# Kernel optimization log

Hardware: AMD Instinct MI355X
Metric: run time of the kernel (lower is better)

Reference implementation:

```python
import jax, jax.numpy as jnp
import numpy as np

N_NODES = 10000
IN_CH = 128
OUT_CH = 128
N_EDGES = 320000


def setup_inputs() -> dict:
    key = jax.random.key(0)
    k1, k2, k3, k4 = jax.random.split(key, 4)
    x = jax.random.normal(k1, (N_NODES, IN_CH), dtype=jnp.float32)
    edge_index = jax.random.randint(k2, (N_EDGES, 2), 0, N_NODES, dtype=jnp.int64)
    # Linear weights (torch stores [out, in]); scale like kaiming-uniform-ish
    w = jax.random.normal(k3, (OUT_CH, IN_CH), dtype=jnp.float32) / np.sqrt(IN_CH)
    b = jax.random.normal(k4, (OUT_CH, IN_CH), dtype=jnp.float32) / np.sqrt(IN_CH)
    return {"x": x, "edge_index": edge_index, "w": w, "b": b}


def reference(x, edge_index, w, b):
    n = x.shape[0]
    # Each edge (i, j) contributes x[j] to node i and x[i] to node j (undirected).
    src = jnp.concatenate([edge_index[:, 1], edge_index[:, 0]])  # feature source
    dst = jnp.concatenate([edge_index[:, 0], edge_index[:, 1]])  # aggregation target
    # segment-sum of gathered neighbor features -> [n, in_ch]
    agg_sum = jax.ops.segment_sum(x[src], dst, num_segments=n)
    deg = jax.ops.segment_sum(jnp.ones_like(dst, dtype=x.dtype), dst, num_segments=n)
    # mean with zero fallback for isolated nodes (original uses zeros vector)
    agg = jnp.where(deg[:, None] > 0, agg_sum / jnp.maximum(deg, 1.0)[:, None], 0.0)
    # out = ReLU(agg @ w^T + x @ b^T)
    return jax.nn.relu(agg @ w.T + x @ b.T)
```

## Files before the change

kernel.cpp:

```cpp
#include <hip/hip_runtime.h>

#define N_NODES 10000
#define CH 128
#define N_EDGES 320000
#define CAP 128
#define CSTR 16

#define NSLICE 8
#define FILL_CHUNKS (N_EDGES / 256)
#define FILL_BLOCKS (FILL_CHUNKS * NSLICE)
#define CONV_THREADS (N_NODES * CH / 8)
#define CONV_BLOCKS ((CONV_THREADS + 255) / 256)
#define PACK_THREADS (128 * 128)
#define PACK_BLOCKS (PACK_THREADS / 256)
#define KSEG 5
#define WBK (KSEG * CH)


typedef __attribute__((ext_vector_type(8))) short short8v;
typedef __attribute__((ext_vector_type(4))) float floatx4;

__device__ __forceinline__ unsigned short f2bf(float f) {
    unsigned u = __float_as_uint(f);
    return (unsigned short)((u + 0x7FFFu + ((u >> 16) & 1u)) >> 16);
}
__device__ __forceinline__ float bf2f(unsigned short h) {
    return __uint_as_float(((unsigned)h) << 16);
}

__global__ __launch_bounds__(256) void fill_conv_pack_kernel(const int* __restrict__ ei,
                                                             int* __restrict__ cursor,
                                                             unsigned short* __restrict__ adj,
                                                             const float* __restrict__ x,
                                                             unsigned short* __restrict__ xhi,
                                                             unsigned short* __restrict__ xlo,
                                                             const float* __restrict__ w,
                                                             const float* __restrict__ b,
                                                             unsigned short* __restrict__ wbt)
{
    const int bid = blockIdx.x;
    if (bid < FILL_BLOCKS) {
        const int slice = bid & (NSLICE - 1);
        const int chunk = bid >> 3;
        const int t = chunk * 256 + threadIdx.x;
        const int2 p = ((const int2*)ei)[t];
        const int a = p.x, c = p.y;
        const bool aok = (unsigned)a < N_NODES && (unsigned)c < N_NODES;
        if (aok && (a & 7) == slice) {
            const int s0 = atomicAdd(&cursor[a * CSTR], 1);
            if (s0 < CAP) adj[(size_t)a * CAP + s0] = (unsigned short)c;
        }
        if (aok && (c & 7) == slice) {
            const int s1 = atomicAdd(&cursor[c * CSTR], 1);
            if (s1 < CAP) adj[(size_t)c * CAP + s1] = (unsigned short)a;
        }
    } else if (bid < FILL_BLOCKS + CONV_BLOCKS) {
        const int t = (bid - FILL_BLOCKS) * 256 + threadIdx.x;
        const float4 a = ((const float4*)x)[t * 2];
        const float4 c = ((const float4*)x)[t * 2 + 1];
        ushort4 h0, h1, l0, l1;
        h0.x = f2bf(a.x); l0.x = f2bf(a.x - bf2f(h0.x));
        h0.y = f2bf(a.y); l0.y = f2bf(a.y - bf2f(h0.y));
        h0.z = f2bf(a.z); l0.z = f2bf(a.z - bf2f(h0.z));
        h0.w = f2bf(a.w); l0.w = f2bf(a.w - bf2f(h0.w));
        h1.x = f2bf(c.x); l1.x = f2bf(c.x - bf2f(h1.x));
        h1.y = f2bf(c.y); l1.y = f2bf(c.y - bf2f(h1.y));
        h1.z = f2bf(c.z); l1.z = f2bf(c.z - bf2f(h1.z));
        h1.w = f2bf(c.w); l1.w = f2bf(c.w - bf2f(h1.w));
        ((ushort4*)xhi)[t * 2]     = h0;
        ((ushort4*)xhi)[t * 2 + 1] = h1;
        ((ushort4*)xlo)[t * 2]     = l0;
        ((ushort4*)xlo)[t * 2 + 1] = l1;
    } else {
        const int t = (bid - FILL_BLOCKS - CONV_BLOCKS) * 256 + threadIdx.x;
        const int n = t >> 7;
        const int k = t & 127;
        const float wv = w[n * CH + k];
        const float bv = b[n * CH + k];
        const unsigned short whi = f2bf(wv);
        const unsigned short wlo = f2bf(wv - bf2f(whi));
        const unsigned short bhi = f2bf(bv);
        const unsigned short blo = f2bf(bv - bf2f(bhi));
        unsigned short* row = wbt + (size_t)n * WBK;
        row[k]          = whi;
        row[CH + k]     = wlo;
        row[2 * CH + k] = bhi;
        row[3 * CH + k] = blo;
        row[4 * CH + k] = bhi;
    }
}

__global__ __launch_bounds__(256) void gather_kernel(const unsigned short* __restrict__ xhi,
                                                     const int* __restrict__ cursor,
                                                     const unsigned short* __restrict__ adj,
                                                     unsigned short* __restrict__ aggb)
{
    const int wv   = threadIdx.x >> 6;
    const int node = blockIdx.x * 4 + wv;
    const int lane = threadIdx.x & 63;
    const int h    = lane >> 4;
    const int l    = lane & 15;

    const int deg = cursor[node * CSTR];
    const int d   = deg < CAP ? deg : CAP;
    const unsigned short* nb = adj + (size_t)node * CAP;

    float4 accA = {0.f, 0.f, 0.f, 0.f};
    float4 accB = {0.f, 0.f, 0.f, 0.f};
    const int nit = (d + 3) >> 2;
#pragma unroll 4
    for (int it = 0; it < nit; ++it) {
        const int idx = 4 * it + h;
        int j = nb[idx];
        j = j < N_NODES ? j : 0;
        const uint4 q = ((const uint4*)(xhi + (size_t)j * CH))[l];
        const float m = idx < d ? 1.0f : 0.0f;
        accA.x += m * __uint_as_float(q.x << 16);
        accA.y += m * __uint_as_float(q.x & 0xffff0000u);
        accA.z += m * __uint_as_float(q.y << 16);
        accA.w += m * __uint_as_float(q.y & 0xffff0000u);
        accB.x += m * __uint_as_float(q.z << 16);
        accB.y += m * __uint_as_float(q.z & 0xffff0000u);
        accB.z += m * __uint_as_float(q.w << 16);
        accB.w += m * __uint_as_float(q.w & 0xffff0000u);
    }
    accA.x += __shfl_xor(accA.x, 16, 64);
    accA.y += __shfl_xor(accA.y, 16, 64);
    accA.z += __shfl_xor(accA.z, 16, 64);
    accA.w += __shfl_xor(accA.w, 16, 64);
    accB.x += __shfl_xor(accB.x, 16, 64);
    accB.y += __shfl_xor(accB.y, 16, 64);
    accB.z += __shfl_xor(accB.z, 16, 64);
    accB.w += __shfl_xor(accB.w, 16, 64);
    accA.x += __shfl_xor(accA.x, 32, 64);
    accA.y += __shfl_xor(accA.y, 32, 64);
    accA.z += __shfl_xor(accA.z, 32, 64);
    accA.w += __shfl_xor(accA.w, 32, 64);
    accB.x += __shfl_xor(accB.x, 32, 64);
    accB.y += __shfl_xor(accB.y, 32, 64);
    accB.z += __shfl_xor(accB.z, 32, 64);
    accB.w += __shfl_xor(accB.w, 32, 64);

    if (h == 0) {
        const float inv = deg > 0 ? 1.0f / (float)deg : 0.0f;
        uint4 o;
        o.x = (unsigned)f2bf(accA.x * inv) | ((unsigned)f2bf(accA.y * inv) << 16);
        o.y = (unsigned)f2bf(accA.z * inv) | ((unsigned)f2bf(accA.w * inv) << 16);
        o.z = (unsigned)f2bf(accB.x * inv) | ((unsigned)f2bf(accB.y * inv) << 16);
        o.w = (unsigned)f2bf(accB.z * inv) | ((unsigned)f2bf(accB.w * inv) << 16);
        ((uint4*)(aggb + (size_t)node * CH))[l] = o;
    }
}

__global__ __launch_bounds__(256) void mfma_gemm_kernel(const unsigned short* __restrict__ aggb,
                                                        const unsigned short* __restrict__ xhi,
                                                        const unsigned short* __restrict__ xlo,
                                                        const unsigned short* __restrict__ wbt,
                                                        float* __restrict__ out)
{
    const int wv    = threadIdx.x >> 6;
    const int lane  = threadIdx.x & 63;
    const int W     = blockIdx.x * 4 + wv;
    const int mtile = W >> 3;
    const int n0    = (W & 7) * 16;
    const int r     = lane & 15;
    const int q     = lane >> 4;
    const int arow  = mtile * 16 + r;

    const unsigned short* brow = wbt + (size_t)(n0 + r) * WBK;
    floatx4 acc = {0.f, 0.f, 0.f, 0.f};

#pragma unroll
    for (int seg = 0; seg < KSEG; ++seg) {
        const unsigned short* A = (seg < 2) ? aggb : ((seg < 4) ? xhi : xlo);
        const int wk = seg * CH;
#pragma unroll
        for (int ks = 0; ks < 4; ++ks) {
            const int k0 = ks * 32 + q * 8;
            const short8v af = *(const short8v*)(A + (size_t)arow * CH + k0);
            const short8v bf = *(const short8v*)(brow + wk + k0);
            acc = __builtin_amdgcn_mfma_f32_16x16x32_bf16(af, bf, acc, 0, 0, 0);
        }
    }

    const int mbase = mtile * 16 + q * 4;
#pragma unroll
    for (int rr = 0; rr < 4; ++rr) {
        float v = acc[rr];
        v = v > 0.f ? v : 0.f;
        out[(size_t)(mbase + rr) * CH + n0 + r] = v;
    }
}

extern "C" void kernel_launch(void* const* d_in, const int* in_sizes, int n_in,
                              void* d_out, int out_size, void* d_ws, size_t ws_size,
                              hipStream_t stream)
{
    const float* x  = (const float*)d_in[0];
    const int*   ei = (const int*)d_in[1];
    const float* w  = (const float*)d_in[2];
    const float* b  = (const float*)d_in[3];
    float*       out = (float*)d_out;

    int*            cursor = (int*)d_ws;
    unsigned short* adj    = (unsigned short*)((char*)d_ws + 640000);
    unsigned short* xhi    = (unsigned short*)((char*)d_ws + 3200000);
    unsigned short* xlo    = (unsigned short*)((char*)d_ws + 5760000);
    unsigned short* aggb   = (unsigned short*)((char*)d_ws + 8320000);
    unsigned short* wbt    = (unsigned short*)((char*)d_ws + 10880000);

    hipMemsetAsync(d_ws, 0, (size_t)N_NODES * CSTR * sizeof(int), stream);

    fill_conv_pack_kernel<<<FILL_BLOCKS + CONV_BLOCKS + PACK_BLOCKS, 256, 0, stream>>>(
        ei, cursor, adj, x, xhi, xlo, w, b, wbt);
    gather_kernel<<<N_NODES / 4, 256, 0, stream>>>(xhi, cursor, adj, aggb);
    mfma_gemm_kernel<<<1250, 256, 0, stream>>>(aggb, xhi, xlo, wbt, out);
}
```

Before: 126.1 us.

## Fuse neighbor gather into MFMA GEMM via shared-memory aggregate tile

```diff
diff --git a/kernel.cpp b/kernel.cpp
--- a/kernel.cpp
+++ b/kernel.cpp
@@ -15,6 +15,8 @@
 #define PACK_BLOCKS (PACK_THREADS / 256)
 #define KSEG 5
 #define WBK (KSEG * CH)
+#define NPB2 16
+#define AP 136
 
 
 typedef __attribute__((ext_vector_type(8))) short short8v;
@@ -39,23 +41,8 @@
                                                              unsigned short* __restrict__ wbt)
 {
     const int bid = blockIdx.x;
-    if (bid < FILL_BLOCKS) {
-        const int slice = bid & (NSLICE - 1);
-        const int chunk = bid >> 3;
-        const int t = chunk * 256 + threadIdx.x;
-        const int2 p = ((const int2*)ei)[t];
-        const int a = p.x, c = p.y;
-        const bool aok = (unsigned)a < N_NODES && (unsigned)c < N_NODES;
-        if (aok && (a & 7) == slice) {
-            const int s0 = atomicAdd(&cursor[a * CSTR], 1);
-            if (s0 < CAP) adj[(size_t)a * CAP + s0] = (unsigned short)c;
-        }
-        if (aok && (c & 7) == slice) {
-            const int s1 = atomicAdd(&cursor[c * CSTR], 1);
-            if (s1 < CAP) adj[(size_t)c * CAP + s1] = (unsigned short)a;
-        }
-    } else if (bid < FILL_BLOCKS + CONV_BLOCKS) {
-        const int t = (bid - FILL_BLOCKS) * 256 + threadIdx.x;
+    if (bid < CONV_BLOCKS) {
+        const int t = bid * 256 + threadIdx.x;
         const float4 a = ((const float4*)x)[t * 2];
         const float4 c = ((const float4*)x)[t * 2 + 1];
         ushort4 h0, h1, l0, l1;
@@ -71,8 +58,24 @@
         ((ushort4*)xhi)[t * 2 + 1] = h1;
         ((ushort4*)xlo)[t * 2]     = l0;
         ((ushort4*)xlo)[t * 2 + 1] = l1;
+    } else if (bid < CONV_BLOCKS + FILL_BLOCKS) {
+        const int fb    = bid - CONV_BLOCKS;
+        const int slice = fb & (NSLICE - 1);
+        const int chunk = fb >> 3;
+        const int t = chunk * 256 + threadIdx.x;
+        const int2 p = ((const int2*)ei)[t];
+        const int a = p.x, c = p.y;
+        const bool aok = (unsigned)a < N_NODES && (unsigned)c < N_NODES;
+        if (aok && (a & 7) == slice) {
+            const int s0 = atomicAdd(&cursor[a * CSTR], 1);
+            if (s0 < CAP) adj[(size_t)a * CAP + s0] = (unsigned short)c;
+        }
+        if (aok && (c & 7) == slice) {
+            const int s1 = atomicAdd(&cursor[c * CSTR], 1);
+            if (s1 < CAP) adj[(size_t)c * CAP + s1] = (unsigned short)a;
+        }
     } else {
-        const int t = (bid - FILL_BLOCKS - CONV_BLOCKS) * 256 + threadIdx.x;
+        const int t = (bid - CONV_BLOCKS - FILL_BLOCKS) * 256 + threadIdx.x;
         const int n = t >> 7;
         const int k = t & 127;
         const float wv = w[n * CH + k];
@@ -90,100 +93,104 @@
     }
 }
 
-__global__ __launch_bounds__(256) void gather_kernel(const unsigned short* __restrict__ xhi,
-                                                     const int* __restrict__ cursor,
-                                                     const unsigned short* __restrict__ adj,
-                                                     unsigned short* __restrict__ aggb)
+__global__ __launch_bounds__(512) void gather_mfma_kernel(const unsigned short* __restrict__ xhi,
+                                                          const unsigned short* __restrict__ xlo,
+                                                          const int* __restrict__ cursor,
+                                                          const unsigned short* __restrict__ adj,
+                                                          const unsigned short* __restrict__ wbt,
+                                                          float* __restrict__ out)
 {
-    const int wv   = threadIdx.x >> 6;
-    const int node = blockIdx.x * 4 + wv;
-    const int lane = threadIdx.x & 63;
-    const int h    = lane >> 4;
-    const int l    = lane & 15;
-
-    const int deg = cursor[node * CSTR];
-    const int d   = deg < CAP ? deg : CAP;
-    const unsigned short* nb = adj + (size_t)node * CAP;
-
-    float4 accA = {0.f, 0.f, 0.f, 0.f};
-    float4 accB = {0.f, 0.f, 0.f, 0.f};
-    const int nit = (d + 3) >> 2;
+    __shared__ unsigned short sh_a[NPB2 * AP];
+    const int tid   = threadIdx.x;
+    const int wv    = tid >> 6;
+    const int lane  = tid & 63;
+    const int node0 = blockIdx.x * NPB2;
+
+    const int h = lane >> 4;
+    const int l = lane & 15;
+
+#pragma unroll
+    for (int i = 0; i < 2; ++i) {
+        const int nl   = wv * 2 + i;
+        const int node = node0 + nl;
+        const int deg  = cursor[node * CSTR];
+        const int d    = deg < CAP ? deg : CAP;
+        const unsigned short* nb = adj + (size_t)node * CAP;
+
+        float4 accA = {0.f, 0.f, 0.f, 0.f};
+        float4 accB = {0.f, 0.f, 0.f, 0.f};
+        const int nit = (d + 3) >> 2;
 #pragma unroll 4
-    for (int it = 0; it < nit; ++it) {
-        const int idx = 4 * it + h;
-        int j = nb[idx];
-        j = j < N_NODES ? j : 0;
-        const uint4 q = ((const uint4*)(xhi + (size_t)j * CH))[l];
-        const float m = idx < d ? 1.0f : 0.0f;
-        accA.x += m * __uint_as_float(q.x << 16);
-        accA.y += m * __uint_as_float(q.x & 0xffff0000u);
-        accA.z += m * __uint_as_float(q.y << 16);
-        accA.w += m * __uint_as_float(q.y & 0xffff0000u);
-        accB.x += m * __uint_as_float(q.z << 16);
-        accB.y += m * __uint_as_float(q.z & 0xffff0000u);
-        accB.z += m * __uint_as_float(q.w << 16);
-        accB.w += m * __uint_as_float(q.w & 0xffff0000u);
-    }
-    accA.x += __shfl_xor(accA.x, 16, 64);
-    accA.y += __shfl_xor(accA.y, 16, 64);
-    accA.z += __shfl_xor(accA.z, 16, 64);
-    accA.w += __shfl_xor(accA.w, 16, 64);
-    accB.x += __shfl_xor(accB.x, 16, 64);
-    accB.y += __shfl_xor(accB.y, 16, 64);
-    accB.z += __shfl_xor(accB.z, 16, 64);
-    accB.w += __shfl_xor(accB.w, 16, 64);
-    accA.x += __shfl_xor(accA.x, 32, 64);
-    accA.y += __shfl_xor(accA.y, 32, 64);
-    accA.z += __shfl_xor(accA.z, 32, 64);
-    accA.w += __shfl_xor(accA.w, 32, 64);
-    accB.x += __shfl_xor(accB.x, 32, 64);
-    accB.y += __shfl_xor(accB.y, 32, 64);
-    accB.z += __shfl_xor(accB.z, 32, 64);
-    accB.w += __shfl_xor(accB.w, 32, 64);
-
-    if (h == 0) {
-        const float inv = deg > 0 ? 1.0f / (float)deg : 0.0f;
-        uint4 o;
-        o.x = (unsigned)f2bf(accA.x * inv) | ((unsigned)f2bf(accA.y * inv) << 16);
-        o.y = (unsigned)f2bf(accA.z * inv) | ((unsigned)f2bf(accA.w * inv) << 16);
-        o.z = (unsigned)f2bf(accB.x * inv) | ((unsigned)f2bf(accB.y * inv) << 16);
-        o.w = (unsigned)f2bf(accB.z * inv) | ((unsigned)f2bf(accB.w * inv) << 16);
-        ((uint4*)(aggb + (size_t)node * CH))[l] = o;
-    }
-}
-
-__global__ __launch_bounds__(256) void mfma_gemm_kernel(const unsigned short* __restrict__ aggb,
-                                                        const unsigned short* __restrict__ xhi,
-                                                        const unsigned short* __restrict__ xlo,
-                                                        const unsigned short* __restrict__ wbt,
-                                                        float* __restrict__ out)
-{
-    const int wv    = threadIdx.x >> 6;
-    const int lane  = threadIdx.x & 63;
-    const int W     = blockIdx.x * 4 + wv;
-    const int mtile = W >> 3;
-    const int n0    = (W & 7) * 16;
-    const int r     = lane & 15;
-    const int q     = lane >> 4;
-    const int arow  = mtile * 16 + r;
-
+        for (int it = 0; it < nit; ++it) {
+            const int idx = 4 * it + h;
+            int j = nb[idx];
+            j = j < N_NODES ? j : 0;
+            const uint4 q = ((const uint4*)(xhi + (size_t)j * CH))[l];
+            const float m = idx < d ? 1.0f : 0.0f;
+            accA.x += m * __uint_as_float(q.x << 16);
+            accA.y += m * __uint_as_float(q.x & 0xffff0000u);
+            accA.z += m * __uint_as_float(q.y << 16);
+            accA.w += m * __uint_as_float(q.y & 0xffff0000u);
+            accB.x += m * __uint_as_float(q.z << 16);
+            accB.y += m * __uint_as_float(q.z & 0xffff0000u);
+            accB.z += m * __uint_as_float(q.w << 16);
+            accB.w += m * __uint_as_float(q.w & 0xffff0000u);
+        }
+        accA.x += __shfl_xor(accA.x, 16, 64);
+        accA.y += __shfl_xor(accA.y, 16, 64);
+        accA.z += __shfl_xor(accA.z, 16, 64);
+        accA.w += __shfl_xor(accA.w, 16, 64);
+        accB.x += __shfl_xor(accB.x, 16, 64);
+        accB.y += __shfl_xor(accB.y, 16, 64);
+        accB.z += __shfl_xor(accB.z, 16, 64);
+        accB.w += __shfl_xor(accB.w, 16, 64);
+        accA.x += __shfl_xor(accA.x, 32, 64);
+        accA.y += __shfl_xor(accA.y, 32, 64);
+        accA.z += __shfl_xor(accA.z, 32, 64);
+        accA.w += __shfl_xor(accA.w, 32, 64);
+        accB.x += __shfl_xor(accB.x, 32, 64);
+        accB.y += __shfl_xor(accB.y, 32, 64);
+        accB.z += __shfl_xor(accB.z, 32, 64);
+        accB.w += __shfl_xor(accB.w, 32, 64);
+
+        if (h == 0) {
+            const float inv = deg > 0 ? 1.0f / (float)deg : 0.0f;
+            uint4 o;
+            o.x = (unsigned)f2bf(accA.x * inv) | ((unsigned)f2bf(accA.y * inv) << 16);
+            o.y = (unsigned)f2bf(accA.z * inv) | ((unsigned)f2bf(accA.w * inv) << 16);
+            o.z = (unsigned)f2bf(accB.x * inv) | ((unsigned)f2bf(accB.y * inv) << 16);
+            o.w = (unsigned)f2bf(accB.z * inv) | ((unsigned)f2bf(accB.w * inv) << 16);
+            ((uint4*)(sh_a + (size_t)nl * AP))[l] = o;
+        }
+    }
+    __syncthreads();
+
+    const int r  = lane & 15;
+    const int q  = lane >> 4;
+    const int n0 = wv * 16;
     const unsigned short* brow = wbt + (size_t)(n0 + r) * WBK;
     floatx4 acc = {0.f, 0.f, 0.f, 0.f};
 
 #pragma unroll
     for (int seg = 0; seg < KSEG; ++seg) {
-        const unsigned short* A = (seg < 2) ? aggb : ((seg < 4) ? xhi : xlo);
         const int wk = seg * CH;
 #pragma unroll
         for (int ks = 0; ks < 4; ++ks) {
             const int k0 = ks * 32 + q * 8;
-            const short8v af = *(const short8v*)(A + (size_t)arow * CH + k0);
+            short8v af;
+            if (seg < 2) {
+                af = *(const short8v*)(sh_a + (size_t)r * AP + k0);
+            } else if (seg < 4) {
+                af = *(const short8v*)(xhi + (size_t)(node0 + r) * CH + k0);
+            } else {
+                af = *(const short8v*)(xlo + (size_t)(node0 + r) * CH + k0);
+            }
             const short8v bf = *(const short8v*)(brow + wk + k0);
             acc = __builtin_amdgcn_mfma_f32_16x16x32_bf16(af, bf, acc, 0, 0, 0);
         }
     }
 
-    const int mbase = mtile * 16 + q * 4;
+    const int mbase = node0 + q * 4;
 #pragma unroll
     for (int rr = 0; rr < 4; ++rr) {
         float v = acc[rr];
@@ -206,13 +213,11 @@
     unsigned short* adj    = (unsigned short*)((char*)d_ws + 640000);
     unsigned short* xhi    = (unsigned short*)((char*)d_ws + 3200000);
     unsigned short* xlo    = (unsigned short*)((char*)d_ws + 5760000);
-    unsigned short* aggb   = (unsigned short*)((char*)d_ws + 8320000);
-    unsigned short* wbt    = (unsigned short*)((char*)d_ws + 10880000);
+    unsigned short* wbt    = (unsigned short*)((char*)d_ws + 8320000);
 
     hipMemsetAsync(d_ws, 0, (size_t)N_NODES * CSTR * sizeof(int), stream);
 
-    fill_conv_pack_kernel<<<FILL_BLOCKS + CONV_BLOCKS + PACK_BLOCKS, 256, 0, stream>>>(
+    fill_conv_pack_kernel<<<CONV_BLOCKS + FILL_BLOCKS + PACK_BLOCKS, 256, 0, stream>>>(
         ei, cursor, adj, x, xhi, xlo, w, b, wbt);
-    gather_kernel<<<N_NODES / 4, 256, 0, stream>>>(xhi, cursor, adj, aggb);
-    mfma_gemm_kernel<<<1250, 256, 0, stream>>>(aggb, xhi, xlo, wbt, out);
-}
+    gather_mfma_kernel<<<N_NODES / NPB2, 512, 0, stream>>>(xhi, xlo, cursor, adj, wbt, out);
+}
```

Result: no change. 124.9 us (-0.9%).
